# Optimization experiments

Hardware: AMD Instinct MI355X
Metric: run time of the kernel (lower is better)

## Reference

```python
import jax, jax.numpy as jnp
import numpy as np

B, N, IN_DIM, OUT_DIM, H = 4, 2048, 1024, 1024, 16
HEAD_DIM = OUT_DIM // H  # 64


def setup_inputs() -> dict:
    key = jax.random.key(0)
    k_x, k_q, k_k, k_v, k_o = jax.random.split(key, 5)
    s = 1.0 / np.sqrt(IN_DIM)
    return {
        "x": jax.random.normal(k_x, (B, N, IN_DIM), dtype=jnp.float32),
        "w_q": jax.random.normal(k_q, (IN_DIM, OUT_DIM), dtype=jnp.float32) * s,
        "w_k": jax.random.normal(k_k, (IN_DIM, OUT_DIM), dtype=jnp.float32) * s,
        "w_v": jax.random.normal(k_v, (IN_DIM, OUT_DIM), dtype=jnp.float32) * s,
        "w_out": jax.random.normal(k_o, (OUT_DIM, OUT_DIM), dtype=jnp.float32) * s,
    }


def reference(x, w_q, w_k, w_v, w_out):
    b, n, _ = x.shape
    scale = 1.0 / jnp.sqrt(jnp.float32(HEAD_DIM))
    # QKV projections, split into heads: [b, h, n, d]
    q = (x @ w_q).reshape(b, n, H, HEAD_DIM).transpose(0, 2, 1, 3)
    k = (x @ w_k).reshape(b, n, H, HEAD_DIM).transpose(0, 2, 1, 3)
    v = (x @ w_v).reshape(b, n, H, HEAD_DIM).transpose(0, 2, 1, 3)
    # full score matrix [b, h, q, k]
    scores = jnp.einsum("bhqd,bhkd->bhqk", q, k) * scale
    # NOTE: source applies softmax over dim=1 (the HEAD axis) — reproduce exactly
    attn = jax.nn.softmax(scores, axis=1)
    # dropout p=0.0 -> identity
    ctx = jnp.einsum("bhqk,bhkd->bqhd", attn, v).reshape(b, n, OUT_DIM)
    return ctx @ w_out
```

## Files before the change

kernel.cpp:

```cpp
#include <hip/hip_runtime.h>
#include <hip/hip_bf16.h>

typedef unsigned short u16;
typedef unsigned int u32;
typedef __attribute__((ext_vector_type(8))) short short8;
typedef __attribute__((ext_vector_type(4))) float float4v;
typedef __attribute__((ext_vector_type(4))) unsigned int uint4v;

__device__ __forceinline__ u16 f2bf(float f) {
    union { float f; unsigned int u; } v; v.f = f;
    unsigned int r = v.u + 0x7fffu + ((v.u >> 16) & 1u);
    return (u16)(r >> 16);
}
__device__ __forceinline__ float bf2f(u16 h) {
    union { unsigned int u; float f; } v; v.u = ((unsigned int)h) << 16;
    return v.f;
}

__device__ __forceinline__ void gld_lds16(const u16* g, u16* l) {
    __builtin_amdgcn_global_load_lds(
        (const __attribute__((address_space(1))) u32*)g,
        (__attribute__((address_space(3))) u32*)l, 16, 0, 0);
}

__global__ __launch_bounds__(256) void convert_x(
    const float* __restrict__ x, u16* __restrict__ xb) {
    int i = (blockIdx.x * 256 + threadIdx.x) * 8;
    float4v a = *(const float4v*)&x[i];
    float4v b = *(const float4v*)&x[i + 4];
    u16 tmp[8] __attribute__((aligned(16)));
#pragma unroll
    for (int j = 0; j < 4; ++j) { tmp[j] = f2bf(a[j]); tmp[4 + j] = f2bf(b[j]); }
    *(uint4v*)&xb[i] = *(uint4v*)tmp;
}

__global__ __launch_bounds__(256) void transpose_w(
    const float* __restrict__ w0, const float* __restrict__ w1,
    const float* __restrict__ w2, const float* __restrict__ w3,
    u16* __restrict__ wqkv, u16* __restrict__ wout) {
    __shared__ u16 t[32][33];
    int z = blockIdx.z;
    const float* w = (z == 0) ? w0 : (z == 1) ? w1 : (z == 2) ? w2 : w3;
    u16* o = (z == 3) ? wout : (wqkv + (size_t)z * 1024 * 1024);
    int bx = blockIdx.x * 32;
    int by = blockIdx.y * 32;
    int x = threadIdx.x, y = threadIdx.y;
#pragma unroll
    for (int i = 0; i < 4; ++i)
        t[y + i * 8][x] = f2bf(w[(size_t)(by + y + i * 8) * 1024 + bx + x]);
    __syncthreads();
#pragma unroll
    for (int i = 0; i < 4; ++i)
        o[(size_t)(bx + y + i * 8) * 1024 + by + x] = t[x][y + i * 8];
}

__global__ __launch_bounds__(256) void gemm_qkv(
    const u16* __restrict__ A, const u16* __restrict__ Bt,
    u16* __restrict__ Q, u16* __restrict__ Kb, u16* __restrict__ Vt, int K) {
    __shared__ __attribute__((aligned(16))) u16 As[128 * 32];
    __shared__ __attribute__((aligned(16))) u16 Bs[128 * 32];
    const int tid = threadIdx.x;
    const int m0 = blockIdx.y * 128;
    const int n0 = blockIdx.x * 128;
    const int wid = tid >> 6;
    const int lane = tid & 63;
    const int ln = lane & 15, kq = lane >> 4;
    const int wm = (wid >> 1) * 64, wn = (wid & 1) * 64;

    float4v acc[4][4] = {};
    for (int k0 = 0; k0 < K; k0 += 32) {
#pragma unroll
        for (int i = 0; i < 2; ++i) {
            int chunk = tid + i * 256;
            int row = chunk >> 2, cg = chunk & 3;
            u16* lA = &As[(size_t)(i * 256 + wid * 64) * 8];
            u16* lB = &Bs[(size_t)(i * 256 + wid * 64) * 8];
            gld_lds16(&A[(size_t)(m0 + row) * K + k0 + cg * 8], lA);
            gld_lds16(&Bt[(size_t)(n0 + row) * K + k0 + cg * 8], lB);
        }
        __syncthreads();
        short8 af[4], bfr[4];
#pragma unroll
        for (int mt = 0; mt < 4; ++mt)
            af[mt] = *(const short8*)&As[(wm + mt * 16 + ln) * 32 + kq * 8];
#pragma unroll
        for (int nt = 0; nt < 4; ++nt)
            bfr[nt] = *(const short8*)&Bs[(wn + nt * 16 + ln) * 32 + kq * 8];
#pragma unroll
        for (int mt = 0; mt < 4; ++mt)
#pragma unroll
            for (int nt = 0; nt < 4; ++nt)
                acc[mt][nt] = __builtin_amdgcn_mfma_f32_16x16x32_bf16(
                    af[mt], bfr[nt], acc[mt][nt], 0, 0, 0);
        __syncthreads();
    }
    if (n0 < 2048) {
        u16* C = (n0 < 1024) ? Q : Kb;
        int nb = n0 & 1023;
#pragma unroll
        for (int mt = 0; mt < 4; ++mt)
#pragma unroll
            for (int nt = 0; nt < 4; ++nt)
#pragma unroll
                for (int r = 0; r < 4; ++r) {
                    int row = m0 + wm + mt * 16 + kq * 4 + r;
                    int col = nb + wn + nt * 16 + ln;
                    C[(size_t)row * 1024 + col] = f2bf(acc[mt][nt][r]);
                }
    } else {
#pragma unroll
        for (int mt = 0; mt < 4; ++mt)
#pragma unroll
            for (int nt = 0; nt < 4; ++nt)
#pragma unroll
                for (int r = 0; r < 4; ++r) {
                    int t = m0 + wm + mt * 16 + kq * 4 + r;
                    int col = (n0 - 2048) + wn + nt * 16 + ln;
                    int b = t >> 11, n = t & 2047;
                    Vt[((size_t)(b * 1024 + col)) * 2048 + n] = f2bf(acc[mt][nt][r]);
                }
    }
}

__global__ __launch_bounds__(256) void gemm_out(
    const u16* __restrict__ A, const u16* __restrict__ Bt,
    float* __restrict__ C, int N, int K) {
    __shared__ __attribute__((aligned(16))) u16 As[128 * 32];
    __shared__ __attribute__((aligned(16))) u16 Bs[128 * 32];
    const int tid = threadIdx.x;
    const int m0 = blockIdx.y * 128;
    const int n0 = blockIdx.x * 128;
    const int wid = tid >> 6;
    const int lane = tid & 63;
    const int ln = lane & 15, kq = lane >> 4;
    const int wm = (wid >> 1) * 64, wn = (wid & 1) * 64;

    float4v acc[4][4] = {};
    for (int k0 = 0; k0 < K; k0 += 32) {
#pragma unroll
        for (int i = 0; i < 2; ++i) {
            int chunk = tid + i * 256;
            int row = chunk >> 2, cg = chunk & 3;
            u16* lA = &As[(size_t)(i * 256 + wid * 64) * 8];
            u16* lB = &Bs[(size_t)(i * 256 + wid * 64) * 8];
            gld_lds16(&A[(size_t)(m0 + row) * K + k0 + cg * 8], lA);
            gld_lds16(&Bt[(size_t)(n0 + row) * K + k0 + cg * 8], lB);
        }
        __syncthreads();
        short8 af[4], bfr[4];
#pragma unroll
        for (int mt = 0; mt < 4; ++mt)
            af[mt] = *(const short8*)&As[(wm + mt * 16 + ln) * 32 + kq * 8];
#pragma unroll
        for (int nt = 0; nt < 4; ++nt)
            bfr[nt] = *(const short8*)&Bs[(wn + nt * 16 + ln) * 32 + kq * 8];
#pragma unroll
        for (int mt = 0; mt < 4; ++mt)
#pragma unroll
            for (int nt = 0; nt < 4; ++nt)
                acc[mt][nt] = __builtin_amdgcn_mfma_f32_16x16x32_bf16(
                    af[mt], bfr[nt], acc[mt][nt], 0, 0, 0);
        __syncthreads();
    }
#pragma unroll
    for (int mt = 0; mt < 4; ++mt)
#pragma unroll
        for (int nt = 0; nt < 4; ++nt)
#pragma unroll
            for (int r = 0; r < 4; ++r) {
                int row = m0 + wm + mt * 16 + kq * 4 + r;
                int col = n0 + wn + nt * 16 + ln;
                C[(size_t)row * N + col] = acc[mt][nt][r];
            }
}

__global__ __launch_bounds__(1024) void attn_kernel(
    const u16* __restrict__ qb, const u16* __restrict__ kb,
    const u16* __restrict__ vt, u32* __restrict__ ctx) {
    __shared__ __attribute__((aligned(16))) u16 E[2][16 * 32 * 40];
    __shared__ float Di[32 * 36];

    const int bid = blockIdx.x;
    const int b  = (bid >> 1) & 3;
    const int kh = bid & 1;
    const int q0 = (bid >> 3) * 32;
    const int tid = threadIdx.x;
    const int wid = tid >> 6, lane = tid & 63;
    const int ln = lane & 15, kq = lane >> 4;
    const int h = wid;

    short8 aq[2][2];
#pragma unroll
    for (int mt = 0; mt < 2; ++mt)
#pragma unroll
        for (int kc = 0; kc < 2; ++kc)
            aq[mt][kc] = *(const short8*)&qb[
                (size_t)(b * 2048 + q0 + mt * 16 + ln) * 1024 +
                h * 64 + kc * 32 + kq * 8];

    float4v cacc[2][4] = {};

    const int kbeg = kh * 1024, kend = kbeg + 1024;
#pragma unroll 1
    for (int kt = kbeg; kt < kend; kt += 32) {
        const int cur = (kt >> 5) & 1;
        short8 bk[2][2];
        short8 bv[4];
#pragma unroll
        for (int kc = 0; kc < 2; ++kc)
#pragma unroll
            for (int nt = 0; nt < 2; ++nt)
                bk[kc][nt] = *(const short8*)&kb[
                    (size_t)(b * 2048 + kt + nt * 16 + ln) * 1024 +
                    h * 64 + kc * 32 + kq * 8];
#pragma unroll
        for (int nt = 0; nt < 4; ++nt)
            bv[nt] = *(const short8*)&vt[
                (size_t)(b * 1024 + h * 64 + nt * 16 + ln) * 2048 + kt + kq * 8];

        float4v sacc[2][2] = {};
#pragma unroll
        for (int kc = 0; kc < 2; ++kc)
#pragma unroll
            for (int mt = 0; mt < 2; ++mt)
#pragma unroll
                for (int nt = 0; nt < 2; ++nt)
                    sacc[mt][nt] = __builtin_amdgcn_mfma_f32_16x16x32_bf16(
                        aq[mt][kc], bk[kc][nt], sacc[mt][nt], 0, 0, 0);

#pragma unroll
        for (int mt = 0; mt < 2; ++mt)
#pragma unroll
            for (int nt = 0; nt < 2; ++nt)
#pragma unroll
                for (int r = 0; r < 4; ++r) {
                    float s = sacc[mt][nt][r] * 0.18033688f;
                    E[cur][(h * 32 + mt * 16 + kq * 4 + r) * 40 + nt * 16 + ln] =
                        f2bf(exp2f(fminf(s, 115.0f)));
                }
        __syncthreads();

        {
            int q = tid >> 5, kk = tid & 31;
            float d = 0.f;
#pragma unroll
            for (int hh = 0; hh < 16; ++hh)
                d += bf2f(E[cur][(hh * 32 + q) * 40 + kk]);
            Di[q * 36 + kk] = __builtin_amdgcn_rcpf(d);
        }
        __syncthreads();

        short8 ap[2];
#pragma unroll
        for (int mt = 0; mt < 2; ++mt) {
            const u16* ep = &E[cur][(h * 32 + mt * 16 + ln) * 40 + kq * 8];
            const float* dp = &Di[(mt * 16 + ln) * 36 + kq * 8];
            u16 tmp[8] __attribute__((aligned(16)));
#pragma unroll
            for (int j = 0; j < 8; ++j)
                tmp[j] = f2bf(bf2f(ep[j]) * dp[j]);
            ap[mt] = *(short8*)tmp;
        }
#pragma unroll
        for (int nt = 0; nt < 4; ++nt)
#pragma unroll
            for (int mt = 0; mt < 2; ++mt)
                cacc[mt][nt] = __builtin_amdgcn_mfma_f32_16x16x32_bf16(
                    ap[mt], bv[nt], cacc[mt][nt], 0, 0, 0);
    }

#pragma unroll
    for (int mt = 0; mt < 2; ++mt)
#pragma unroll
        for (int nt = 0; nt < 4; ++nt)
#pragma unroll
            for (int r = 0; r < 4; ++r) {
                float v = cacc[mt][nt][r];
                float v2 = __shfl_xor(v, 1);
                if ((lane & 1) == 0) {
                    int row = b * 2048 + q0 + mt * 16 + kq * 4 + r;
                    int col = h * 64 + nt * 16 + ln;
                    u32* addr = &ctx[((size_t)row * 1024 + col) >> 1];
                    u32 old = __hip_atomic_load(addr, __ATOMIC_RELAXED,
                                                __HIP_MEMORY_SCOPE_AGENT);
                    u32 assumed;
                    do {
                        assumed = old;
                        float lo = bf2f((u16)(assumed & 0xffff)) + v;
                        float hi = bf2f((u16)(assumed >> 16)) + v2;
                        u32 nv = ((u32)f2bf(hi) << 16) | (u32)f2bf(lo);
                        old = atomicCAS(addr, assumed, nv);
                    } while (old != assumed);
                }
            }
}

extern "C" void kernel_launch(void* const* d_in, const int* in_sizes, int n_in,
                              void* d_out, int out_size, void* d_ws, size_t ws_size,
                              hipStream_t stream) {
    const float* x   = (const float*)d_in[0];
    const float* w_q = (const float*)d_in[1];
    const float* w_k = (const float*)d_in[2];
    const float* w_v = (const float*)d_in[3];
    const float* w_o = (const float*)d_in[4];

    char* ws = (char*)d_ws;
    const size_t SZ_TOK = (size_t)8192 * 1024 * 2;
    u16* x_bf   = (u16*)(ws);
    u16* ctx    = (u16*)(ws);
    u16* wqkv_t = (u16*)(ws + SZ_TOK);
    u16* wto    = (u16*)(ws + SZ_TOK + (size_t)3 * 1024 * 1024 * 2);
    u16* q_buf  = (u16*)(ws + SZ_TOK + (size_t)4 * 1024 * 1024 * 2);
    u16* k_buf  = (u16*)d_out;
    u16* vt_buf = (u16*)d_out + (size_t)8192 * 1024;

    convert_x<<<4096, 256, 0, stream>>>(x, x_bf);

    transpose_w<<<dim3(32, 32, 4), dim3(32, 8), 0, stream>>>(
        w_q, w_k, w_v, w_o, wqkv_t, wto);

    gemm_qkv<<<dim3(24, 64), 256, 0, stream>>>(
        x_bf, wqkv_t, q_buf, k_buf, vt_buf, 1024);

    hipMemsetAsync(ctx, 0, SZ_TOK, stream);
    attn_kernel<<<512, 1024, 0, stream>>>(q_buf, k_buf, vt_buf, (u32*)ctx);

    gemm_out<<<dim3(8, 64), 256, 0, stream>>>(ctx, wto, (float*)d_out, 1024, 1024);
}
```

Before: 547.4 us.

## Drop key-split atomics in attention, keep exp scores in fp32, prefetch K

The attention kernel no longer splits the key range across two blocks, so the bf16 CAS-loop atomic accumulation and the memset of ctx are removed. Each block now walks all 2048 keys and writes ctx directly. Exp scores are kept in fp32 in LDS and the head-axis reduction is vectorized over 256 threads. The next K tile is prefetched into registers and the probability pack uses truncation. In exchange the grid shrinks from 512 to 256 blocks of 1024 threads, the serial loop per block doubles in length, and LDS use grows.

```diff
diff --git a/kernel.cpp b/kernel.cpp
--- a/kernel.cpp
+++ b/kernel.cpp
@@ -12,9 +12,11 @@
     unsigned int r = v.u + 0x7fffu + ((v.u >> 16) & 1u);
     return (u16)(r >> 16);
 }
-__device__ __forceinline__ float bf2f(u16 h) {
-    union { unsigned int u; float f; } v; v.u = ((unsigned int)h) << 16;
-    return v.f;
+__device__ __forceinline__ u32 fbits(float f) {
+    union { float f; u32 u; } v; v.f = f; return v.u;
+}
+__device__ __forceinline__ u32 pack_bf2_trunc(float a, float b) {
+    return (fbits(a) >> 16) | (fbits(b) & 0xffff0000u);
 }
 
 __device__ __forceinline__ void gld_lds16(const u16* g, u16* l) {
@@ -176,14 +178,12 @@
 
 __global__ __launch_bounds__(1024) void attn_kernel(
     const u16* __restrict__ qb, const u16* __restrict__ kb,
-    const u16* __restrict__ vt, u32* __restrict__ ctx) {
-    __shared__ __attribute__((aligned(16))) u16 E[2][16 * 32 * 40];
+    const u16* __restrict__ vt, u16* __restrict__ cb) {
+    __shared__ float E[2][16 * 32 * 36];
     __shared__ float Di[32 * 36];
 
-    const int bid = blockIdx.x;
-    const int b  = (bid >> 1) & 3;
-    const int kh = bid & 1;
-    const int q0 = (bid >> 3) * 32;
+    const int b = blockIdx.y;
+    const int q0 = blockIdx.x * 32;
     const int tid = threadIdx.x;
     const int wid = tid >> 6, lane = tid & 63;
     const int ln = lane & 15, kq = lane >> 4;
@@ -200,18 +200,27 @@
 
     float4v cacc[2][4] = {};
 
-    const int kbeg = kh * 1024, kend = kbeg + 1024;
+    short8 bk_cur[2][2], bk_nxt[2][2];
+#pragma unroll
+    for (int kc = 0; kc < 2; ++kc)
+#pragma unroll
+        for (int nt = 0; nt < 2; ++nt)
+            bk_cur[kc][nt] = *(const short8*)&kb[
+                (size_t)(b * 2048 + 0 + nt * 16 + ln) * 1024 +
+                h * 64 + kc * 32 + kq * 8];
+
 #pragma unroll 1
-    for (int kt = kbeg; kt < kend; kt += 32) {
+    for (int kt = 0; kt < 2048; kt += 32) {
         const int cur = (kt >> 5) & 1;
-        short8 bk[2][2];
+        const int ktn = (kt + 32 < 2048) ? kt + 32 : 0;
+
         short8 bv[4];
 #pragma unroll
         for (int kc = 0; kc < 2; ++kc)
 #pragma unroll
             for (int nt = 0; nt < 2; ++nt)
-                bk[kc][nt] = *(const short8*)&kb[
-                    (size_t)(b * 2048 + kt + nt * 16 + ln) * 1024 +
+                bk_nxt[kc][nt] = *(const short8*)&kb[
+                    (size_t)(b * 2048 + ktn + nt * 16 + ln) * 1024 +
                     h * 64 + kc * 32 + kq * 8];
 #pragma unroll
         for (int nt = 0; nt < 4; ++nt)
@@ -226,7 +235,7 @@
 #pragma unroll
                 for (int nt = 0; nt < 2; ++nt)
                     sacc[mt][nt] = __builtin_amdgcn_mfma_f32_16x16x32_bf16(
-                        aq[mt][kc], bk[kc][nt], sacc[mt][nt], 0, 0, 0);
+                        aq[mt][kc], bk_cur[kc][nt], sacc[mt][nt], 0, 0, 0);
 
 #pragma unroll
         for (int mt = 0; mt < 2; ++mt)
@@ -235,31 +244,41 @@
 #pragma unroll
                 for (int r = 0; r < 4; ++r) {
                     float s = sacc[mt][nt][r] * 0.18033688f;
-                    E[cur][(h * 32 + mt * 16 + kq * 4 + r) * 40 + nt * 16 + ln] =
-                        f2bf(exp2f(fminf(s, 115.0f)));
+                    E[cur][(h * 32 + mt * 16 + kq * 4 + r) * 36 + nt * 16 + ln] =
+                        exp2f(fminf(s, 115.0f));
                 }
         __syncthreads();
 
-        {
-            int q = tid >> 5, kk = tid & 31;
-            float d = 0.f;
+        if (tid < 256) {
+            int q = tid >> 3, k4 = (tid & 7) * 4;
+            float4v s4 = {};
 #pragma unroll
             for (int hh = 0; hh < 16; ++hh)
-                d += bf2f(E[cur][(hh * 32 + q) * 40 + kk]);
-            Di[q * 36 + kk] = __builtin_amdgcn_rcpf(d);
+                s4 += *(const float4v*)&E[cur][(hh * 32 + q) * 36 + k4];
+            float4v r4;
+#pragma unroll
+            for (int j = 0; j < 4; ++j) r4[j] = __builtin_amdgcn_rcpf(s4[j]);
+            *(float4v*)&Di[q * 36 + k4] = r4;
         }
         __syncthreads();
 
         short8 ap[2];
 #pragma unroll
         for (int mt = 0; mt < 2; ++mt) {
-            const u16* ep = &E[cur][(h * 32 + mt * 16 + ln) * 40 + kq * 8];
+            const float* ep = &E[cur][(h * 32 + mt * 16 + ln) * 36 + kq * 8];
             const float* dp = &Di[(mt * 16 + ln) * 36 + kq * 8];
-            u16 tmp[8] __attribute__((aligned(16)));
-#pragma unroll
-            for (int j = 0; j < 8; ++j)
-                tmp[j] = f2bf(bf2f(ep[j]) * dp[j]);
-            ap[mt] = *(short8*)tmp;
+            float4v e0 = *(const float4v*)ep;
+            float4v e1 = *(const float4v*)(ep + 4);
+            float4v d0 = *(const float4v*)dp;
+            float4v d1 = *(const float4v*)(dp + 4);
+            float4v p0 = e0 * d0, p1 = e1 * d1;
+            uint4v w;
+            w.x = pack_bf2_trunc(p0.x, p0.y);
+            w.y = pack_bf2_trunc(p0.z, p0.w);
+            w.z = pack_bf2_trunc(p1.x, p1.y);
+            w.w = pack_bf2_trunc(p1.z, p1.w);
+            union { uint4v u; short8 s; } cvt; cvt.u = w;
+            ap[mt] = cvt.s;
         }
 #pragma unroll
         for (int nt = 0; nt < 4; ++nt)
@@ -267,6 +286,12 @@
             for (int mt = 0; mt < 2; ++mt)
                 cacc[mt][nt] = __builtin_amdgcn_mfma_f32_16x16x32_bf16(
                     ap[mt], bv[nt], cacc[mt][nt], 0, 0, 0);
+
+#pragma unroll
+        for (int kc = 0; kc < 2; ++kc)
+#pragma unroll
+            for (int nt = 0; nt < 2; ++nt)
+                bk_cur[kc][nt] = bk_nxt[kc][nt];
     }
 
 #pragma unroll
@@ -275,23 +300,9 @@
         for (int nt = 0; nt < 4; ++nt)
 #pragma unroll
             for (int r = 0; r < 4; ++r) {
-                float v = cacc[mt][nt][r];
-                float v2 = __shfl_xor(v, 1);
-                if ((lane & 1) == 0) {
-                    int row = b * 2048 + q0 + mt * 16 + kq * 4 + r;
-                    int col = h * 64 + nt * 16 + ln;
-                    u32* addr = &ctx[((size_t)row * 1024 + col) >> 1];
-                    u32 old = __hip_atomic_load(addr, __ATOMIC_RELAXED,
-                                                __HIP_MEMORY_SCOPE_AGENT);
-                    u32 assumed;
-                    do {
-                        assumed = old;
-                        float lo = bf2f((u16)(assumed & 0xffff)) + v;
-                        float hi = bf2f((u16)(assumed >> 16)) + v2;
-                        u32 nv = ((u32)f2bf(hi) << 16) | (u32)f2bf(lo);
-                        old = atomicCAS(addr, assumed, nv);
-                    } while (old != assumed);
-                }
+                int row = b * 2048 + q0 + mt * 16 + kq * 4 + r;
+                int col = h * 64 + nt * 16 + ln;
+                cb[(size_t)row * 1024 + col] = f2bf(cacc[mt][nt][r]);
             }
 }
 
@@ -322,8 +333,7 @@
     gemm_qkv<<<dim3(24, 64), 256, 0, stream>>>(
         x_bf, wqkv_t, q_buf, k_buf, vt_buf, 1024);
 
-    hipMemsetAsync(ctx, 0, SZ_TOK, stream);
-    attn_kernel<<<512, 1024, 0, stream>>>(q_buf, k_buf, vt_buf, (u32*)ctx);
+    attn_kernel<<<dim3(64, 4), 1024, 0, stream>>>(q_buf, k_buf, vt_buf, ctx);
 
     gemm_out<<<dim3(8, 64), 256, 0, stream>>>(ctx, wto, (float*)d_out, 1024, 1024);
 }
```

Result: no change. 539.9 us (-1.4%).
